# Kernel optimization log

Hardware: AMD Instinct MI355X
Metric: run time of the kernel (lower is better)

## Reference

```python
import jax, jax.numpy as jnp
import numpy as np

N = 32768
E = 524288
B = 128
D = 256


def setup_inputs() -> dict:
    key = jax.random.key(0)
    ks = jax.random.split(key, 8)
    b_z = jax.random.normal(ks[0], (N, D), dtype=jnp.float32)
    src = jax.random.randint(ks[1], (E,), 0, N, dtype=jnp.int32)
    dst = jax.random.randint(ks[2], (E,), 0, N, dtype=jnp.int32)
    b_edge_weight = jax.random.uniform(ks[3], (E,), dtype=jnp.float32)
    # Glorot-ish init for layer weights (256->128->64->1)
    W1 = jax.random.normal(ks[4], (256, 128), dtype=jnp.float32) / np.sqrt(256)
    W2 = jax.random.normal(ks[5], (128, 64), dtype=jnp.float32) / np.sqrt(128)
    W3 = jax.random.normal(ks[6], (64, 1), dtype=jnp.float32) / np.sqrt(64)
    b1 = jnp.zeros((128,), jnp.float32)
    b2 = jnp.zeros((64,), jnp.float32)
    b3 = jnp.zeros((1,), jnp.float32)
    return {"b_z": b_z, "src": src, "dst": dst, "b_edge_weight": b_edge_weight,
            "W1": W1, "b1": b1, "W2": W2, "b2": b2, "W3": W3, "b3": b3,
            "b_size": B}


def _degree_norms(src, dst, n):
    ones = jnp.ones(src.shape[0], jnp.float32)
    out_deg = jax.ops.segment_sum(ones, src, num_segments=n)
    in_deg = jax.ops.segment_sum(ones, dst, num_segments=n)
    # DGL GraphConv norm='both': unweighted degrees, clamped to 1
    return jnp.clip(out_deg, 1.0) ** -0.5, jnp.clip(in_deg, 1.0) ** -0.5


def _gcn_layer(x, src, dst, ew, norm_src, norm_dst, W, b, use_tanh):
    # norm='both': scale source features, transform first (in_feats > out_feats),
    # weighted neighbor sum, then scale by in-degree norm, add bias, activate.
    h = (x * norm_src[:, None]) @ W            # [N, out]
    m = h[src] * ew[:, None]                   # [E, out] gathered messages
    agg = jax.ops.segment_sum(m, dst, num_segments=x.shape[0])  # [N, out]
    out = agg * norm_dst[:, None] + b
    return jnp.tanh(out) if use_tanh else out


def reference(b_z, src, dst, b_edge_weight, W1, b1, W2, b2, W3, b3, b_size):
    norm_src, norm_dst = _degree_norms(src, dst, b_z.shape[0])
    h = _gcn_layer(b_z, src, dst, b_edge_weight, norm_src, norm_dst, W1, b1, True)
    h = _gcn_layer(h, src, dst, b_edge_weight, norm_src, norm_dst, W2, b2, True)
    h = _gcn_layer(h, src, dst, b_edge_weight, norm_src, norm_dst, W3, b3, False)
    return h.reshape(b_size, -1)
```

## Files before the change

kernel.cpp:

```cpp
#include <hip/hip_runtime.h>


#define NB 256
#define NW4 8192
#define RSEG 8

typedef unsigned int uint32;
typedef unsigned char uchar_t;
typedef unsigned short ushort_t;
typedef __attribute__((ext_vector_type(8))) short bf16x8;
typedef __attribute__((ext_vector_type(4))) float f32x4;

__device__ inline ushort_t f2bf(float f) {
  uint32 u = __float_as_uint(f);
  u += 0x7fffu + ((u >> 16) & 1u);
  return (ushort_t)(u >> 16);
}
__device__ inline float bf2f(ushort_t h) { return __uint_as_float(((uint32)h) << 16); }

__device__ inline float fast_tanh(float x) {
  float xc = fminf(fmaxf(x, -30.f), 30.f);
  float t = __expf(2.0f * xc);
  return (t - 1.0f) * __builtin_amdgcn_rcpf(t + 1.0f);
}

__global__ __launch_bounds__(1024) void hist_wsplit_kernel(
    const int* __restrict__ src, const int* __restrict__ dst, uint32* __restrict__ part,
    const float* __restrict__ W1, const float* __restrict__ W2,
    ushort_t* __restrict__ WhT1, ushort_t* __restrict__ WlT1,
    ushort_t* __restrict__ WhT2, int e, int epb) {
  const int t = threadIdx.x;
  if (blockIdx.x >= NB) {
    int i = (blockIdx.x - NB) * 1024 + t;
    if (i < 256 * 128) {
      int k = i / 128, c = i % 128;
      float f = W1[i];
      ushort_t h = f2bf(f);
      WhT1[(size_t)c * 256 + k] = h;
      WlT1[(size_t)c * 256 + k] = f2bf(f - bf2f(h));
    } else if (i < 256 * 128 + 128 * 64) {
      int j = i - 256 * 128;
      int k = j / 64, c = j % 64;
      WhT2[(size_t)c * 128 + k] = f2bf(W2[j]);
    }
    return;
  }
  __shared__ uint32 hs[NW4];
  __shared__ uint32 hd[NW4];
  for (int w = t; w < NW4; w += 1024) {
    hs[w] = 0;
    hd[w] = 0;
  }
  __syncthreads();
  const int base = blockIdx.x * epb;
  for (int k = t; k < epb; k += 1024) {
    int i = base + k;
    if (i < e) {
      int s = src[i], d = dst[i];
      atomicAdd(&hs[s >> 2], 1u << ((s & 3) * 8));
      atomicAdd(&hd[d >> 2], 1u << ((d & 3) * 8));
    }
  }
  __syncthreads();
  uint32* ps = part + (size_t)blockIdx.x * NW4;
  uint32* pd = part + (size_t)(NB + blockIdx.x) * NW4;
  for (int w = t; w < NW4; w += 1024) {
    ps[w] = hs[w];
    pd[w] = hd[w];
  }
}

__global__ __launch_bounds__(256) void norm_partial(const uint32* __restrict__ part,
                                                    uint32* __restrict__ psum, int n4) {
  const int w = blockIdx.x * 256 + threadIdx.x;
  const int seg = blockIdx.y;
  const int a = blockIdx.z;
  const uint32* p = part + (size_t)a * NB * n4 + (size_t)seg * (NB / RSEG) * n4 + w;
  uint32 s = 0;
#pragma unroll
  for (int r = 0; r < NB / RSEG; ++r) s += p[(size_t)r * n4];
  psum[(size_t)a * RSEG * n4 + (size_t)seg * n4 + w] = s;
}

__global__ __launch_bounds__(256) void norm_final(const uint32* __restrict__ psum,
                                                  float* __restrict__ norm_src,
                                                  float* __restrict__ norm_dst,
                                                  int* __restrict__ in_deg,
                                                  int* __restrict__ block_sums, int n4) {
  const int w = blockIdx.x * 256 + threadIdx.x;
  if (w >= n4) return;
  uint32 ss = 0, sd = 0;
#pragma unroll
  for (int seg = 0; seg < RSEG; ++seg) {
    ss += psum[(size_t)seg * n4 + w];
    sd += psum[(size_t)(RSEG + seg) * n4 + w];
  }
  int idsum = 0;
#pragma unroll
  for (int j = 0; j < 4; ++j) {
    int v = w * 4 + j;
    int od = (ss >> (j * 8)) & 0xff;
    int id = (sd >> (j * 8)) & 0xff;
    norm_src[v] = 1.0f / sqrtf((float)max(od, 1));
    norm_dst[v] = 1.0f / sqrtf((float)max(id, 1));
    in_deg[v] = id;
    idsum += id;
  }
#pragma unroll
  for (int off = 32; off > 0; off >>= 1) idsum += __shfl_down(idsum, off, 64);
  if ((threadIdx.x & 63) == 0) block_sums[w >> 6] = idsum;
}

__global__ __launch_bounds__(256) void scan_write_goffs(const int* __restrict__ in_deg,
                                                        const int* __restrict__ block_sums,
                                                        const uint32* __restrict__ part_dst,
                                                        int* __restrict__ row_ptr,
                                                        uchar_t* __restrict__ gpre, int n) {
  __shared__ int sh[256];
  __shared__ int s_boff;
  const int t = threadIdx.x;
  const int gid = blockIdx.x * 256 + t;
  {
    int v = (t < blockIdx.x && t < 128) ? block_sums[t] : 0;
#pragma unroll
    for (int off = 32; off > 0; off >>= 1) v += __shfl_down(v, off, 64);
    if ((t & 63) == 0) sh[t >> 6] = v;
    __syncthreads();
    if (t == 0) s_boff = sh[0] + sh[1] + sh[2] + sh[3];
    __syncthreads();
  }
  int d = (gid < n) ? in_deg[gid] : 0;
  sh[t] = d;
  __syncthreads();
  for (int off = 1; off < 256; off <<= 1) {
    int v = sh[t];
    int add = (t >= off) ? sh[t - off] : 0;
    __syncthreads();
    sh[t] = v + add;
    __syncthreads();
  }
  if (gid >= n) return;
  int excl = s_boff + sh[t] - d;
  row_ptr[gid] = excl;
  if (gid == n - 1) row_ptr[n] = excl + d;
  const int w = gid >> 2;
  const int shft = (gid & 3) * 8;
  const int n4 = n >> 2;
  int cum = 0;
#pragma unroll 8
  for (int r = 0; r < NB; ++r) {
    gpre[(size_t)r * n + gid] = (uchar_t)cum;
    cum += (part_dst[(size_t)r * n4 + w] >> shft) & 0xff;
  }
}

__global__ __launch_bounds__(1024) void scatter_kernel(const int* __restrict__ src,
                                                       const int* __restrict__ dst,
                                                       const float* __restrict__ ew,
                                                       const float* __restrict__ norm_src,
                                                       const int* __restrict__ row_ptr,
                                                       const uchar_t* __restrict__ gpre,
                                                       int2* __restrict__ csr,
                                                       int n, int e, int epb) {
  __shared__ uint32 rk[NW4];
  const int t = threadIdx.x;
  for (int w = t; w < NW4; w += 1024) rk[w] = 0;
  __syncthreads();
  const int base = blockIdx.x * epb;
  const uchar_t* gp = gpre + (size_t)blockIdx.x * n;
  for (int k = t; k < epb; k += 1024) {
    int i = base + k;
    if (i < e) {
      int s = src[i];
      int d = dst[i];
      uint32 sh = (d & 3) * 8;
      uint32 old = atomicAdd(&rk[d >> 2], 1u << sh);
      int rank = (old >> sh) & 0xff;
      int pos = row_ptr[d] + (int)gp[d] + rank;
      csr[pos] = make_int2(s, __float_as_int(ew[i] * norm_src[s]));
    }
  }
}

template <int K, int OUT>
__global__ __launch_bounds__(256) void gemm_mfma(const float* __restrict__ x,
                                                 const ushort_t* __restrict__ WhT,
                                                 const ushort_t* __restrict__ WlT,
                                                 ushort_t* __restrict__ ht, int n) {
  constexpr int BK = 64, KP = BK + 8;
  constexpr int NCT = OUT / 32;
  constexpr int NWLD = OUT * 16 / 256;
  __shared__ ushort_t Xh[64][KP];
  __shared__ ushort_t Wh[OUT][KP], Wl[OUT][KP];

  const int tid = threadIdx.x;
  const int wv = tid >> 6;
  const int lane = tid & 63;
  const int wr = wv >> 1;
  const int wc = wv & 1;
  const int row0 = blockIdx.x * 64;
  const int fr = lane & 15;
  const int fg = lane >> 4;

  f32x4 acc[2][NCT];
#pragma unroll
  for (int i = 0; i < 2; ++i)
#pragma unroll
    for (int j = 0; j < NCT; ++j) acc[i][j] = (f32x4){0.f, 0.f, 0.f, 0.f};

  float4 xr[4];
  ushort4 wrh[NWLD], wrl[NWLD];

#define LOADX(kg)                                                                       \
  {                                                                                     \
    _Pragma("unroll") for (int p_ = 0; p_ < 4; ++p_) {                                  \
      int idx_ = p_ * 256 + tid;                                                        \
      xr[p_] = *reinterpret_cast<const float4*>(                                        \
          x + (size_t)(row0 + (idx_ >> 4)) * K + (kg) + (idx_ & 15) * 4);               \
    }                                                                                   \
  }
#define LOADW(kg)                                                                       \
  {                                                                                     \
    _Pragma("unroll") for (int p_ = 0; p_ < NWLD; ++p_) {                               \
      int idx_ = p_ * 256 + tid;                                                        \
      int c_ = idx_ >> 4, k4_ = idx_ & 15;                                              \
      wrh[p_] = *reinterpret_cast<const ushort4*>(WhT + (size_t)c_ * K + (kg) + k4_ * 4);\
      wrl[p_] = *reinterpret_cast<const ushort4*>(WlT + (size_t)c_ * K + (kg) + k4_ * 4);\
    }                                                                                   \
  }

  LOADX(0);
  LOADW(0);

#pragma unroll 1
  for (int k0 = 0; k0 < K; k0 += BK) {
    __syncthreads();
#pragma unroll
    for (int p = 0; p < 4; ++p) {
      int idx = p * 256 + tid;
      int r = idx >> 4, c4 = idx & 15;
      float4 v = xr[p];
      ushort4 h;
      h.x = f2bf(v.x);
      h.y = f2bf(v.y);
      h.z = f2bf(v.z);
      h.w = f2bf(v.w);
      *reinterpret_cast<ushort4*>(&Xh[r][c4 * 4]) = h;
    }
#pragma unroll
    for (int p = 0; p < NWLD; ++p) {
      int idx = p * 256 + tid;
      int c = idx >> 4, k4 = idx & 15;
      *reinterpret_cast<ushort4*>(&Wh[c][k4 * 4]) = wrh[p];
      *reinterpret_cast<ushort4*>(&Wl[c][k4 * 4]) = wrl[p];
    }
    if (k0 + BK < K) {
      LOADX(k0 + BK);
      LOADW(k0 + BK);
    }
    __syncthreads();

#pragma unroll
    for (int s = 0; s < 2; ++s) {
      const int kk = s * 32 + fg * 8;
      bf16x8 ah[2];
#pragma unroll
      for (int i = 0; i < 2; ++i)
        ah[i] = *reinterpret_cast<const bf16x8*>(&Xh[wr * 32 + i * 16 + fr][kk]);
#pragma unroll
      for (int j = 0; j < NCT; ++j) {
        int c = wc * (OUT / 2) + j * 16 + fr;
        bf16x8 bh = *reinterpret_cast<const bf16x8*>(&Wh[c][kk]);
        bf16x8 bl = *reinterpret_cast<const bf16x8*>(&Wl[c][kk]);
#pragma unroll
        for (int i = 0; i < 2; ++i) {
          acc[i][j] = __builtin_amdgcn_mfma_f32_16x16x32_bf16(ah[i], bh, acc[i][j], 0, 0, 0);
          acc[i][j] = __builtin_amdgcn_mfma_f32_16x16x32_bf16(ah[i], bl, acc[i][j], 0, 0, 0);
        }
      }
    }
  }
#undef LOADX
#undef LOADW

#pragma unroll
  for (int i = 0; i < 2; ++i) {
#pragma unroll
    for (int q = 0; q < 4; ++q) {
      int row = row0 + wr * 32 + i * 16 + fg * 4 + q;
#pragma unroll
      for (int j = 0; j < NCT; ++j) {
        int col = wc * (OUT / 2) + j * 16 + fr;
        ht[(size_t)row * OUT + col] = f2bf(acc[i][j][q]);
      }
    }
  }
}

template <int K, int OUT>
__global__ __launch_bounds__(256) void gemm_mfma_bf16in(const ushort_t* __restrict__ x,
                                                        const ushort_t* __restrict__ WhT,
                                                        ushort_t* __restrict__ ht, int n) {
  constexpr int BK = 64, KP = BK + 8;
  constexpr int NCT = OUT / 32;
  constexpr int NWLD = OUT * 16 / 256;
  __shared__ ushort_t Xh[64][KP];
  __shared__ ushort_t Wh[OUT][KP];

  const int tid = threadIdx.x;
  const int wv = tid >> 6;
  const int lane = tid & 63;
  const int wr = wv >> 1;
  const int wc = wv & 1;
  const int row0 = blockIdx.x * 64;
  const int fr = lane & 15;
  const int fg = lane >> 4;

  f32x4 acc[2][NCT];
#pragma unroll
  for (int i = 0; i < 2; ++i)
#pragma unroll
    for (int j = 0; j < NCT; ++j) acc[i][j] = (f32x4){0.f, 0.f, 0.f, 0.f};

  ushort4 xr[4];
  ushort4 wrh[NWLD];

#define LOADX(kg)                                                                       \
  {                                                                                     \
    _Pragma("unroll") for (int p_ = 0; p_ < 4; ++p_) {                                  \
      int idx_ = p_ * 256 + tid;                                                        \
      xr[p_] = *reinterpret_cast<const ushort4*>(                                       \
          x + (size_t)(row0 + (idx_ >> 4)) * K + (kg) + (idx_ & 15) * 4);               \
    }                                                                                   \
  }
#define LOADW(kg)                                                                       \
  {                                                                                     \
    _Pragma("unroll") for (int p_ = 0; p_ < NWLD; ++p_) {                               \
      int idx_ = p_ * 256 + tid;                                                        \
      int c_ = idx_ >> 4, k4_ = idx_ & 15;                                              \
      wrh[p_] = *reinterpret_cast<const ushort4*>(WhT + (size_t)c_ * K + (kg) + k4_ * 4);\
    }                                                                                   \
  }

  LOADX(0);
  LOADW(0);

#pragma unroll 1
  for (int k0 = 0; k0 < K; k0 += BK) {
    __syncthreads();
#pragma unroll
    for (int p = 0; p < 4; ++p) {
      int idx = p * 256 + tid;
      *reinterpret_cast<ushort4*>(&Xh[idx >> 4][(idx & 15) * 4]) = xr[p];
    }
#pragma unroll
    for (int p = 0; p < NWLD; ++p) {
      int idx = p * 256 + tid;
      *reinterpret_cast<ushort4*>(&Wh[idx >> 4][(idx & 15) * 4]) = wrh[p];
    }
    if (k0 + BK < K) {
      LOADX(k0 + BK);
      LOADW(k0 + BK);
    }
    __syncthreads();

#pragma unroll
    for (int s = 0; s < 2; ++s) {
      const int kk = s * 32 + fg * 8;
      bf16x8 ah[2];
#pragma unroll
      for (int i = 0; i < 2; ++i)
        ah[i] = *reinterpret_cast<const bf16x8*>(&Xh[wr * 32 + i * 16 + fr][kk]);
#pragma unroll
      for (int j = 0; j < NCT; ++j) {
        int c = wc * (OUT / 2) + j * 16 + fr;
        bf16x8 bh = *reinterpret_cast<const bf16x8*>(&Wh[c][kk]);
#pragma unroll
        for (int i = 0; i < 2; ++i)
          acc[i][j] = __builtin_amdgcn_mfma_f32_16x16x32_bf16(ah[i], bh, acc[i][j], 0, 0, 0);
      }
    }
  }
#undef LOADX
#undef LOADW

#pragma unroll
  for (int i = 0; i < 2; ++i) {
#pragma unroll
    for (int q = 0; q < 4; ++q) {
      int row = row0 + wr * 32 + i * 16 + fg * 4 + q;
#pragma unroll
      for (int j = 0; j < NCT; ++j) {
        int col = wc * (OUT / 2) + j * 16 + fr;
        ht[(size_t)row * OUT + col] = f2bf(acc[i][j][q]);
      }
    }
  }
}

#define GATHB(e, acc)                                                               \
  {                                                                                 \
    float w_ = __int_as_float(e.y);                                                 \
    ushort4 h_ = *reinterpret_cast<const ushort4*>(ht + (size_t)e.x * OUT + cg * 4);\
    acc.x += w_ * bf2f(h_.x);                                                       \
    acc.y += w_ * bf2f(h_.y);                                                       \
    acc.z += w_ * bf2f(h_.z);                                                       \
    acc.w += w_ * bf2f(h_.w);                                                       \
  }

template <int OUT>
__global__ void aggregate_kernel(const ushort_t* __restrict__ ht, const int* __restrict__ row_ptr,
                                 const int2* __restrict__ csr, const float* __restrict__ norm_dst,
                                 const float* __restrict__ bias, ushort_t* __restrict__ out,
                                 int n) {
  constexpr int LPN = OUT / 4;
  constexpr int NPB = 256 / LPN;
  const int tid = threadIdx.x;
  const int cg = tid % LPN;
  const int v = blockIdx.x * NPB + tid / LPN;
  if (v >= n) return;

  const int s0 = row_ptr[v];
  const int s1 = row_ptr[v + 1];
  float4 a0 = {0, 0, 0, 0}, a1 = {0, 0, 0, 0}, a2 = {0, 0, 0, 0}, a3 = {0, 0, 0, 0};
  int i = s0;
  for (; i + 4 <= s1; i += 4) {
    int2 e0 = csr[i], e1 = csr[i + 1], e2 = csr[i + 2], e3 = csr[i + 3];
    GATHB(e0, a0);
    GATHB(e1, a1);
    GATHB(e2, a2);
    GATHB(e3, a3);
  }
  for (; i < s1; ++i) {
    int2 e = csr[i];
    GATHB(e, a0);
  }
  float nd = norm_dst[v];
  float4 b4 = *reinterpret_cast<const float4*>(bias + cg * 4);
  ushort4 r;
  r.x = f2bf(fast_tanh((a0.x + a1.x + a2.x + a3.x) * nd + b4.x));
  r.y = f2bf(fast_tanh((a0.y + a1.y + a2.y + a3.y) * nd + b4.y));
  r.z = f2bf(fast_tanh((a0.z + a1.z + a2.z + a3.z) * nd + b4.z));
  r.w = f2bf(fast_tanh((a0.w + a1.w + a2.w + a3.w) * nd + b4.w));
  *reinterpret_cast<ushort4*>(out + (size_t)v * OUT + cg * 4) = r;
}

__global__ void aggregate2_fuse3(const ushort_t* __restrict__ ht, const int* __restrict__ row_ptr,
                                 const int2* __restrict__ csr, const float* __restrict__ norm_dst,
                                 const float* __restrict__ bias, const float* __restrict__ W3,
                                 float* __restrict__ ht3, int n) {
  constexpr int OUT = 64;
  constexpr int LPN = OUT / 4;
  constexpr int NPB = 256 / LPN;
  const int tid = threadIdx.x;
  const int cg = tid % LPN;
  const int v = blockIdx.x * NPB + tid / LPN;
  if (v >= n) return;

  const int s0 = row_ptr[v];
  const int s1 = row_ptr[v + 1];
  float4 a0 = {0, 0, 0, 0}, a1 = {0, 0, 0, 0}, a2 = {0, 0, 0, 0}, a3 = {0, 0, 0, 0};
  int i = s0;
  for (; i + 4 <= s1; i += 4) {
    int2 e0 = csr[i], e1 = csr[i + 1], e2 = csr[i + 2], e3 = csr[i + 3];
    GATHB(e0, a0);
    GATHB(e1, a1);
    GATHB(e2, a2);
    GATHB(e3, a3);
  }
  for (; i < s1; ++i) {
    int2 e = csr[i];
    GATHB(e, a0);
  }
  float nd = norm_dst[v];
  float4 b4 = *reinterpret_cast<const float4*>(bias + cg * 4);
  float ox = fast_tanh((a0.x + a1.x + a2.x + a3.x) * nd + b4.x);
  float oy = fast_tanh((a0.y + a1.y + a2.y + a3.y) * nd + b4.y);
  float oz = fast_tanh((a0.z + a1.z + a2.z + a3.z) * nd + b4.z);
  float ow = fast_tanh((a0.w + a1.w + a2.w + a3.w) * nd + b4.w);
  float4 w3 = *reinterpret_cast<const float4*>(W3 + cg * 4);
  float p = ox * w3.x + oy * w3.y + oz * w3.z + ow * w3.w;
#pragma unroll
  for (int m = 1; m < 16; m <<= 1) p += __shfl_xor(p, m, 64);
  if (cg == 0) ht3[v] = p;
}

__global__ void aggregate3_kernel(const float* __restrict__ ht3, const int* __restrict__ row_ptr,
                                  const int2* __restrict__ csr, const float* __restrict__ norm_dst,
                                  const float* __restrict__ b3, float* __restrict__ out, int n) {
  int v = blockIdx.x * blockDim.x + threadIdx.x;
  if (v >= n) return;
  const int s0 = row_ptr[v];
  const int s1 = row_ptr[v + 1];
  float p0 = 0.f, p1 = 0.f, p2 = 0.f, p3 = 0.f;
  int i = s0;
  for (; i + 4 <= s1; i += 4) {
    int2 e0 = csr[i], e1 = csr[i + 1], e2 = csr[i + 2], e3 = csr[i + 3];
    p0 += __int_as_float(e0.y) * ht3[e0.x];
    p1 += __int_as_float(e1.y) * ht3[e1.x];
    p2 += __int_as_float(e2.y) * ht3[e2.x];
    p3 += __int_as_float(e3.y) * ht3[e3.x];
  }
  for (; i < s1; ++i) {
    int2 e = csr[i];
    p0 += __int_as_float(e.y) * ht3[e.x];
  }
  out[v] = (p0 + p1 + p2 + p3) * norm_dst[v] + b3[0];
}

extern "C" void kernel_launch(void* const* d_in, const int* in_sizes, int n_in,
                              void* d_out, int out_size, void* d_ws, size_t ws_size,
                              hipStream_t stream) {
  const float* b_z = (const float*)d_in[0];
  const int* src = (const int*)d_in[1];
  const int* dst = (const int*)d_in[2];
  const float* ew = (const float*)d_in[3];
  const float* W1 = (const float*)d_in[4];
  const float* b1 = (const float*)d_in[5];
  const float* W2 = (const float*)d_in[6];
  const float* b2 = (const float*)d_in[7];
  const float* W3 = (const float*)d_in[8];
  const float* b3 = (const float*)d_in[9];

  const int N = in_sizes[0] / 256;
  const int E = in_sizes[1];
  const int N4 = N / 4;
  const int epb = (E + NB - 1) / NB;

  char* ws = (char*)d_ws;
  size_t off = 0;
  auto alloc = [&](size_t bytes) -> void* {
    void* p = ws + off;
    off += (bytes + 255) & ~(size_t)255;
    return p;
  };

  uint32* part = (uint32*)alloc((size_t)2 * NB * N4 * 4);
  uint32* psum = (uint32*)alloc((size_t)2 * RSEG * N4 * 4);
  uchar_t* gpre = (uchar_t*)alloc((size_t)NB * N);
  float* norm_src = (float*)alloc((size_t)N * 4);
  float* norm_dst = (float*)alloc((size_t)N * 4);
  int* in_deg = (int*)alloc((size_t)N * 4);
  int* row_ptr = (int*)alloc((size_t)(N + 1) * 4);
  int* block_sums = (int*)alloc(256 * 4);
  int2* csr = (int2*)alloc((size_t)E * 8);
  ushort_t* HT = (ushort_t*)alloc((size_t)N * 128 * 2);
  ushort_t* ACT1 = (ushort_t*)alloc((size_t)N * 128 * 2);
  float* HT3 = (float*)alloc((size_t)N * 4);
  ushort_t* WhT1 = (ushort_t*)alloc((size_t)256 * 128 * 2);
  ushort_t* WlT1 = (ushort_t*)alloc((size_t)256 * 128 * 2);
  ushort_t* WhT2 = (ushort_t*)alloc((size_t)128 * 64 * 2);

  const uint32* part_dst = part + (size_t)NB * N4;
  const int nBlocks = (N + 255) / 256;
  const int wsBlocks = (256 * 128 + 128 * 64 + 1023) / 1024;

  hist_wsplit_kernel<<<NB + wsBlocks, 1024, 0, stream>>>(src, dst, part, W1, W2, WhT1, WlT1,
                                                         WhT2, E, epb);
  norm_partial<<<dim3(N4 / 256, RSEG, 2), 256, 0, stream>>>(part, psum, N4);
  norm_final<<<N4 / 256, 256, 0, stream>>>(psum, norm_src, norm_dst, in_deg, block_sums, N4);
  scan_write_goffs<<<nBlocks, 256, 0, stream>>>(in_deg, block_sums, part_dst, row_ptr, gpre, N);
  scatter_kernel<<<NB, 1024, 0, stream>>>(src, dst, ew, norm_src, row_ptr, gpre, csr, N, E, epb);

  gemm_mfma<256, 128><<<N / 64, 256, 0, stream>>>(b_z, WhT1, WlT1, HT, N);
  aggregate_kernel<128><<<(N + 7) / 8, 256, 0, stream>>>(HT, row_ptr, csr, norm_dst, b1, ACT1, N);
  gemm_mfma_bf16in<128, 64><<<N / 64, 256, 0, stream>>>(ACT1, WhT2, HT, N);
  aggregate2_fuse3<<<(N + 15) / 16, 256, 0, stream>>>(HT, row_ptr, csr, norm_dst, b2, W3, HT3, N);
  aggregate3_kernel<<<nBlocks, 256, 0, stream>>>(HT3, row_ptr, csr, norm_dst, b3,
                                                 (float*)d_out, N);
}
```

Before: 105.4 us.

## Fuse graph preprocessing kernels into one cooperative kernel with grid syncs

Measured after the change: 243.4 us. 131% more time.

```diff
diff --git a/kernel.cpp b/kernel.cpp
--- a/kernel.cpp
+++ b/kernel.cpp
@@ -1,4 +1,7 @@
 #include <hip/hip_runtime.h>
+#include <hip/hip_cooperative_groups.h>
+
+namespace cg = cooperative_groups;
 
 
 #define NB 256
@@ -24,160 +27,156 @@
   return (t - 1.0f) * __builtin_amdgcn_rcpf(t + 1.0f);
 }
 
-__global__ __launch_bounds__(1024) void hist_wsplit_kernel(
-    const int* __restrict__ src, const int* __restrict__ dst, uint32* __restrict__ part,
+__global__ __launch_bounds__(1024, 8) void preproc_coop(
+    const int* __restrict__ src, const int* __restrict__ dst, const float* __restrict__ ew,
     const float* __restrict__ W1, const float* __restrict__ W2,
-    ushort_t* __restrict__ WhT1, ushort_t* __restrict__ WlT1,
-    ushort_t* __restrict__ WhT2, int e, int epb) {
+    ushort_t* __restrict__ WhT1, ushort_t* __restrict__ WlT1, ushort_t* __restrict__ WhT2,
+    uint32* __restrict__ part, uint32* __restrict__ psum,
+    float* __restrict__ norm_src, float* __restrict__ norm_dst, int* __restrict__ in_deg,
+    int* __restrict__ block_sums, int* __restrict__ row_ptr, uchar_t* __restrict__ gpre,
+    int2* __restrict__ csr, int n, int e, int epb) {
+  cg::grid_group grid = cg::this_grid();
+  __shared__ uint32 hs[NW4];
+  __shared__ uint32 hd[NW4];
   const int t = threadIdx.x;
-  if (blockIdx.x >= NB) {
-    int i = (blockIdx.x - NB) * 1024 + t;
-    if (i < 256 * 128) {
-      int k = i / 128, c = i % 128;
-      float f = W1[i];
+  const int b = blockIdx.x;
+  const int n4 = n >> 2;
+
+  for (int w = t; w < NW4; w += 1024) {
+    hs[w] = 0;
+    hd[w] = 0;
+  }
+  __syncthreads();
+  {
+    const int base = b * epb;
+    for (int k = t; k < epb; k += 1024) {
+      int i = base + k;
+      if (i < e) {
+        int s = src[i], d = dst[i];
+        atomicAdd(&hs[s >> 2], 1u << ((s & 3) * 8));
+        atomicAdd(&hd[d >> 2], 1u << ((d & 3) * 8));
+      }
+    }
+    __syncthreads();
+    uint32* ps = part + (size_t)b * NW4;
+    uint32* pd = part + (size_t)(NB + b) * NW4;
+    for (int w = t; w < NW4; w += 1024) {
+      ps[w] = hs[w];
+      pd[w] = hd[w];
+    }
+    int j = b * 1024 + t;
+    if (j < 256 * 128) {
+      int k = j / 128, c = j % 128;
+      float f = W1[j];
       ushort_t h = f2bf(f);
       WhT1[(size_t)c * 256 + k] = h;
       WlT1[(size_t)c * 256 + k] = f2bf(f - bf2f(h));
-    } else if (i < 256 * 128 + 128 * 64) {
-      int j = i - 256 * 128;
-      int k = j / 64, c = j % 64;
-      WhT2[(size_t)c * 128 + k] = f2bf(W2[j]);
-    }
-    return;
-  }
-  __shared__ uint32 hs[NW4];
-  __shared__ uint32 hd[NW4];
-  for (int w = t; w < NW4; w += 1024) {
-    hs[w] = 0;
-    hd[w] = 0;
-  }
-  __syncthreads();
-  const int base = blockIdx.x * epb;
-  for (int k = t; k < epb; k += 1024) {
-    int i = base + k;
-    if (i < e) {
-      int s = src[i], d = dst[i];
-      atomicAdd(&hs[s >> 2], 1u << ((s & 3) * 8));
-      atomicAdd(&hd[d >> 2], 1u << ((d & 3) * 8));
-    }
-  }
-  __syncthreads();
-  uint32* ps = part + (size_t)blockIdx.x * NW4;
-  uint32* pd = part + (size_t)(NB + blockIdx.x) * NW4;
-  for (int w = t; w < NW4; w += 1024) {
-    ps[w] = hs[w];
-    pd[w] = hd[w];
-  }
-}
-
-__global__ __launch_bounds__(256) void norm_partial(const uint32* __restrict__ part,
-                                                    uint32* __restrict__ psum, int n4) {
-  const int w = blockIdx.x * 256 + threadIdx.x;
-  const int seg = blockIdx.y;
-  const int a = blockIdx.z;
-  const uint32* p = part + (size_t)a * NB * n4 + (size_t)seg * (NB / RSEG) * n4 + w;
-  uint32 s = 0;
-#pragma unroll
-  for (int r = 0; r < NB / RSEG; ++r) s += p[(size_t)r * n4];
-  psum[(size_t)a * RSEG * n4 + (size_t)seg * n4 + w] = s;
-}
-
-__global__ __launch_bounds__(256) void norm_final(const uint32* __restrict__ psum,
-                                                  float* __restrict__ norm_src,
-                                                  float* __restrict__ norm_dst,
-                                                  int* __restrict__ in_deg,
-                                                  int* __restrict__ block_sums, int n4) {
-  const int w = blockIdx.x * 256 + threadIdx.x;
-  if (w >= n4) return;
-  uint32 ss = 0, sd = 0;
-#pragma unroll
-  for (int seg = 0; seg < RSEG; ++seg) {
-    ss += psum[(size_t)seg * n4 + w];
-    sd += psum[(size_t)(RSEG + seg) * n4 + w];
-  }
-  int idsum = 0;
-#pragma unroll
-  for (int j = 0; j < 4; ++j) {
-    int v = w * 4 + j;
-    int od = (ss >> (j * 8)) & 0xff;
-    int id = (sd >> (j * 8)) & 0xff;
-    norm_src[v] = 1.0f / sqrtf((float)max(od, 1));
-    norm_dst[v] = 1.0f / sqrtf((float)max(id, 1));
-    in_deg[v] = id;
-    idsum += id;
-  }
-#pragma unroll
-  for (int off = 32; off > 0; off >>= 1) idsum += __shfl_down(idsum, off, 64);
-  if ((threadIdx.x & 63) == 0) block_sums[w >> 6] = idsum;
-}
-
-__global__ __launch_bounds__(256) void scan_write_goffs(const int* __restrict__ in_deg,
-                                                        const int* __restrict__ block_sums,
-                                                        const uint32* __restrict__ part_dst,
-                                                        int* __restrict__ row_ptr,
-                                                        uchar_t* __restrict__ gpre, int n) {
-  __shared__ int sh[256];
-  __shared__ int s_boff;
-  const int t = threadIdx.x;
-  const int gid = blockIdx.x * 256 + t;
+    } else if (j < 256 * 128 + 128 * 64) {
+      int jj = j - 256 * 128;
+      int k = jj / 64, c = jj % 64;
+      WhT2[(size_t)c * 128 + k] = f2bf(W2[jj]);
+    }
+  }
+  grid.sync();
+
   {
-    int v = (t < blockIdx.x && t < 128) ? block_sums[t] : 0;
+    int task = b * 1024 + t;
+    const int ntask = 2 * RSEG * n4;
+    if (task < ntask) {
+      int a = task / (RSEG * n4);
+      int rem = task % (RSEG * n4);
+      int seg = rem / n4;
+      int w = rem % n4;
+      const uint32* p = part + (size_t)a * NB * n4 + (size_t)seg * (NB / RSEG) * n4 + w;
+      uint32 s = 0;
+#pragma unroll
+      for (int r = 0; r < NB / RSEG; ++r) s += p[(size_t)r * n4];
+      psum[task] = s;
+    }
+  }
+  grid.sync();
+
+  if (b < 32 && t < 256) {
+    int w = b * 256 + t;
+    uint32 ss = 0, sd = 0;
+#pragma unroll
+    for (int seg = 0; seg < RSEG; ++seg) {
+      ss += psum[(size_t)seg * n4 + w];
+      sd += psum[(size_t)(RSEG + seg) * n4 + w];
+    }
+    int idsum = 0;
+#pragma unroll
+    for (int j = 0; j < 4; ++j) {
+      int v = w * 4 + j;
+      int od = (ss >> (j * 8)) & 0xff;
+      int id = (sd >> (j * 8)) & 0xff;
+      norm_src[v] = 1.0f / sqrtf((float)max(od, 1));
+      norm_dst[v] = 1.0f / sqrtf((float)max(id, 1));
+      in_deg[v] = id;
+      idsum += id;
+    }
+#pragma unroll
+    for (int off = 32; off > 0; off >>= 1) idsum += __shfl_down(idsum, off, 64);
+    if ((t & 63) == 0) block_sums[w >> 6] = idsum;
+  }
+  grid.sync();
+
+  {
+    int* sh = (int*)hs;
+    const bool act = (b < 128);
+    const int gid = b * 256 + (t & 255);
+    int v = (act && t < b && t < 128) ? block_sums[t] : 0;
 #pragma unroll
     for (int off = 32; off > 0; off >>= 1) v += __shfl_down(v, off, 64);
-    if ((t & 63) == 0) sh[t >> 6] = v;
-    __syncthreads();
-    if (t == 0) s_boff = sh[0] + sh[1] + sh[2] + sh[3];
-    __syncthreads();
-  }
-  int d = (gid < n) ? in_deg[gid] : 0;
-  sh[t] = d;
-  __syncthreads();
-  for (int off = 1; off < 256; off <<= 1) {
-    int v = sh[t];
-    int add = (t >= off) ? sh[t - off] : 0;
-    __syncthreads();
-    sh[t] = v + add;
-    __syncthreads();
-  }
-  if (gid >= n) return;
-  int excl = s_boff + sh[t] - d;
-  row_ptr[gid] = excl;
-  if (gid == n - 1) row_ptr[n] = excl + d;
-  const int w = gid >> 2;
-  const int shft = (gid & 3) * 8;
-  const int n4 = n >> 2;
-  int cum = 0;
+    if ((t & 63) == 0) sh[512 + (t >> 6)] = v;
+    __syncthreads();
+    const int s_boff = sh[512] + sh[513];
+    __syncthreads();
+    int d = (act && t < 256 && gid < n) ? in_deg[gid] : 0;
+    if (t < 256) sh[t] = d;
+    __syncthreads();
+    for (int off = 1; off < 256; off <<= 1) {
+      int vv = 0, add = 0;
+      if (t < 256) {
+        vv = sh[t];
+        add = (t >= off) ? sh[t - off] : 0;
+      }
+      __syncthreads();
+      if (t < 256) sh[t] = vv + add;
+      __syncthreads();
+    }
+    if (act && t < 256 && gid < n) {
+      int excl = s_boff + sh[t] - d;
+      row_ptr[gid] = excl;
+      if (gid == n - 1) row_ptr[n] = excl + d;
+      const int w = gid >> 2;
+      const int shft = (gid & 3) * 8;
+      int cum = 0;
 #pragma unroll 8
-  for (int r = 0; r < NB; ++r) {
-    gpre[(size_t)r * n + gid] = (uchar_t)cum;
-    cum += (part_dst[(size_t)r * n4 + w] >> shft) & 0xff;
-  }
-}
-
-__global__ __launch_bounds__(1024) void scatter_kernel(const int* __restrict__ src,
-                                                       const int* __restrict__ dst,
-                                                       const float* __restrict__ ew,
-                                                       const float* __restrict__ norm_src,
-                                                       const int* __restrict__ row_ptr,
-                                                       const uchar_t* __restrict__ gpre,
-                                                       int2* __restrict__ csr,
-                                                       int n, int e, int epb) {
-  __shared__ uint32 rk[NW4];
-  const int t = threadIdx.x;
-  for (int w = t; w < NW4; w += 1024) rk[w] = 0;
-  __syncthreads();
-  const int base = blockIdx.x * epb;
-  const uchar_t* gp = gpre + (size_t)blockIdx.x * n;
-  for (int k = t; k < epb; k += 1024) {
-    int i = base + k;
-    if (i < e) {
-      int s = src[i];
-      int d = dst[i];
-      uint32 sh = (d & 3) * 8;
-      uint32 old = atomicAdd(&rk[d >> 2], 1u << sh);
-      int rank = (old >> sh) & 0xff;
-      int pos = row_ptr[d] + (int)gp[d] + rank;
-      csr[pos] = make_int2(s, __float_as_int(ew[i] * norm_src[s]));
+      for (int r = 0; r < NB; ++r) {
+        gpre[(size_t)r * n + gid] = (uchar_t)cum;
+        cum += (part[(size_t)(NB + r) * n4 + w] >> shft) & 0xff;
+      }
+    }
+  }
+  grid.sync();
+
+  {
+    for (int w = t; w < NW4; w += 1024) hs[w] = 0;
+    __syncthreads();
+    const int base = b * epb;
+    const uchar_t* gp = gpre + (size_t)b * n;
+    for (int k = t; k < epb; k += 1024) {
+      int i = base + k;
+      if (i < e) {
+        int s = src[i];
+        int d = dst[i];
+        uint32 sh2 = (d & 3) * 8;
+        uint32 old = atomicAdd(&hs[d >> 2], 1u << sh2);
+        int rank = (old >> sh2) & 0xff;
+        int pos = row_ptr[d] + (int)gp[d] + rank;
+        csr[pos] = make_int2(s, __float_as_int(ew[i] * norm_src[s]));
+      }
     }
   }
 }
@@ -551,16 +550,15 @@
   ushort_t* WlT1 = (ushort_t*)alloc((size_t)256 * 128 * 2);
   ushort_t* WhT2 = (ushort_t*)alloc((size_t)128 * 64 * 2);
 
-  const uint32* part_dst = part + (size_t)NB * N4;
   const int nBlocks = (N + 255) / 256;
-  const int wsBlocks = (256 * 128 + 128 * 64 + 1023) / 1024;
-
-  hist_wsplit_kernel<<<NB + wsBlocks, 1024, 0, stream>>>(src, dst, part, W1, W2, WhT1, WlT1,
-                                                         WhT2, E, epb);
-  norm_partial<<<dim3(N4 / 256, RSEG, 2), 256, 0, stream>>>(part, psum, N4);
-  norm_final<<<N4 / 256, 256, 0, stream>>>(psum, norm_src, norm_dst, in_deg, block_sums, N4);
-  scan_write_goffs<<<nBlocks, 256, 0, stream>>>(in_deg, block_sums, part_dst, row_ptr, gpre, N);
-  scatter_kernel<<<NB, 1024, 0, stream>>>(src, dst, ew, norm_src, row_ptr, gpre, csr, N, E, epb);
+
+  int n_arg = N, e_arg = E, epb_arg = epb;
+  void* cargs[] = {(void*)&src,      (void*)&dst,        (void*)&ew,       (void*)&W1,
+                   (void*)&W2,       (void*)&WhT1,       (void*)&WlT1,     (void*)&WhT2,
+                   (void*)&part,     (void*)&psum,       (void*)&norm_src, (void*)&norm_dst,
+                   (void*)&in_deg,   (void*)&block_sums, (void*)&row_ptr,  (void*)&gpre,
+                   (void*)&csr,      (void*)&n_arg,      (void*)&e_arg,    (void*)&epb_arg};
+  hipLaunchCooperativeKernel((void*)preproc_coop, dim3(NB), dim3(1024), cargs, 0, stream);
 
   gemm_mfma<256, 128><<<N / 64, 256, 0, stream>>>(b_z, WhT1, WlT1, HT, N);
   aggregate_kernel<128><<<(N + 7) / 8, 256, 0, stream>>>(HT, row_ptr, csr, norm_dst, b1, ACT1, N);
```

## Fuse layer-1 aggregation with layer-2 GEMM into one kernel

Applied to the files above, without the earlier changes.

New measurement: 122.8 us. 16.4% more time.

```diff
diff --git a/kernel.cpp b/kernel.cpp
--- a/kernel.cpp
+++ b/kernel.cpp
@@ -126,7 +126,7 @@
     for (int off = 32; off > 0; off >>= 1) v += __shfl_down(v, off, 64);
     if ((t & 63) == 0) sh[t >> 6] = v;
     __syncthreads();
-    if (t == 0) s_boff = sh[0] + sh[1] + sh[2] + sh[3];
+    if (t == 0) s_boff = sh[0] + sh[1];
     __syncthreads();
   }
   int d = (gid < n) ? in_deg[gid] : 0;
@@ -297,123 +297,129 @@
   }
 }
 
-template <int K, int OUT>
-__global__ __launch_bounds__(256) void gemm_mfma_bf16in(const ushort_t* __restrict__ x,
-                                                        const ushort_t* __restrict__ WhT,
-                                                        ushort_t* __restrict__ ht, int n) {
-  constexpr int BK = 64, KP = BK + 8;
-  constexpr int NCT = OUT / 32;
-  constexpr int NWLD = OUT * 16 / 256;
-  __shared__ ushort_t Xh[64][KP];
-  __shared__ ushort_t Wh[OUT][KP];
+#define GATHB1(e, acc)                                                               \
+  {                                                                                  \
+    float w_ = __int_as_float(e.y);                                                  \
+    ushort4 h_ = *reinterpret_cast<const ushort4*>(ht + (size_t)e.x * 128 + cg * 4); \
+    acc.x += w_ * bf2f(h_.x);                                                        \
+    acc.y += w_ * bf2f(h_.y);                                                        \
+    acc.z += w_ * bf2f(h_.z);                                                        \
+    acc.w += w_ * bf2f(h_.w);                                                        \
+  }
+
+__global__ __launch_bounds__(256) void agg1_gemm2(const ushort_t* __restrict__ ht,
+                                                  const int* __restrict__ row_ptr,
+                                                  const int2* __restrict__ csr,
+                                                  const float* __restrict__ norm_dst,
+                                                  const float* __restrict__ b1,
+                                                  const ushort_t* __restrict__ WhT2,
+                                                  ushort_t* __restrict__ ht2, int n) {
+  constexpr int K = 128, OUT = 64, KP = K + 8;
+  __shared__ ushort_t ACT[64][KP];
+  __shared__ ushort_t WL[OUT][KP];
 
   const int tid = threadIdx.x;
+  const int v0 = blockIdx.x * 64;
+
+#pragma unroll
+  for (int p = 0; p < 8; ++p) {
+    int idx = p * 256 + tid;
+    int c = idx >> 5, k4 = idx & 31;
+    *reinterpret_cast<ushort4*>(&WL[c][k4 * 4]) =
+        *reinterpret_cast<const ushort4*>(WhT2 + (size_t)c * K + k4 * 4);
+  }
+
+  const int cg = tid & 31;
+  const int vsub = tid >> 5;
+#pragma unroll 1
+  for (int p = 0; p < 8; ++p) {
+    const int lv = p * 8 + vsub;
+    const int v = v0 + lv;
+    const int s0 = row_ptr[v];
+    const int s1 = row_ptr[v + 1];
+    float4 a0 = {0, 0, 0, 0}, a1 = {0, 0, 0, 0}, a2 = {0, 0, 0, 0}, a3 = {0, 0, 0, 0};
+    int i = s0;
+    for (; i + 4 <= s1; i += 4) {
+      int2 e0 = csr[i], e1 = csr[i + 1], e2 = csr[i + 2], e3 = csr[i + 3];
+      GATHB1(e0, a0);
+      GATHB1(e1, a1);
+      GATHB1(e2, a2);
+      GATHB1(e3, a3);
+    }
+    for (; i < s1; ++i) {
+      int2 e = csr[i];
+      GATHB1(e, a0);
+    }
+    float nd = norm_dst[v];
+    float4 b4 = *reinterpret_cast<const float4*>(b1 + cg * 4);
+    ushort4 r;
+    r.x = f2bf(fast_tanh((a0.x + a1.x + a2.x + a3.x) * nd + b4.x));
+    r.y = f2bf(fast_tanh((a0.y + a1.y + a2.y + a3.y) * nd + b4.y));
+    r.z = f2bf(fast_tanh((a0.z + a1.z + a2.z + a3.z) * nd + b4.z));
+    r.w = f2bf(fast_tanh((a0.w + a1.w + a2.w + a3.w) * nd + b4.w));
+    *reinterpret_cast<ushort4*>(&ACT[lv][cg * 4]) = r;
+  }
+  __syncthreads();
+
   const int wv = tid >> 6;
   const int lane = tid & 63;
   const int wr = wv >> 1;
   const int wc = wv & 1;
-  const int row0 = blockIdx.x * 64;
   const int fr = lane & 15;
   const int fg = lane >> 4;
 
-  f32x4 acc[2][NCT];
+  f32x4 acc[2][2];
 #pragma unroll
   for (int i = 0; i < 2; ++i)
 #pragma unroll
-    for (int j = 0; j < NCT; ++j) acc[i][j] = (f32x4){0.f, 0.f, 0.f, 0.f};
-
-  ushort4 xr[4];
-  ushort4 wrh[NWLD];
-
-#define LOADX(kg)                                                                       \
-  {                                                                                     \
-    _Pragma("unroll") for (int p_ = 0; p_ < 4; ++p_) {                                  \
-      int idx_ = p_ * 256 + tid;                                                        \
-      xr[p_] = *reinterpret_cast<const ushort4*>(                                       \
-          x + (size_t)(row0 + (idx_ >> 4)) * K + (kg) + (idx_ & 15) * 4);               \
-    }                                                                                   \
-  }
-#define LOADW(kg)                                                                       \
-  {                                                                                     \
-    _Pragma("unroll") for (int p_ = 0; p_ < NWLD; ++p_) {                               \
-      int idx_ = p_ * 256 + tid;                                                        \
-      int c_ = idx_ >> 4, k4_ = idx_ & 15;                                              \
-      wrh[p_] = *reinterpret_cast<const ushort4*>(WhT + (size_t)c_ * K + (kg) + k4_ * 4);\
-    }                                                                                   \
-  }
-
-  LOADX(0);
-  LOADW(0);
-
-#pragma unroll 1
-  for (int k0 = 0; k0 < K; k0 += BK) {
-    __syncthreads();
-#pragma unroll
-    for (int p = 0; p < 4; ++p) {
-      int idx = p * 256 + tid;
-      *reinterpret_cast<ushort4*>(&Xh[idx >> 4][(idx & 15) * 4]) = xr[p];
-    }
-#pragma unroll
-    for (int p = 0; p < NWLD; ++p) {
-      int idx = p * 256 + tid;
-      *reinterpret_cast<ushort4*>(&Wh[idx >> 4][(idx & 15) * 4]) = wrh[p];
-    }
-    if (k0 + BK < K) {
-      LOADX(k0 + BK);
-      LOADW(k0 + BK);
-    }
-    __syncthreads();
-
-#pragma unroll
-    for (int s = 0; s < 2; ++s) {
-      const int kk = s * 32 + fg * 8;
-      bf16x8 ah[2];
+    for (int j = 0; j < 2; ++j) acc[i][j] = (f32x4){0.f, 0.f, 0.f, 0.f};
+
+#pragma unroll
+  for (int s = 0; s < 4; ++s) {
+    const int kk = s * 32 + fg * 8;
+    bf16x8 ah[2];
+#pragma unroll
+    for (int i = 0; i < 2; ++i)
+      ah[i] = *reinterpret_cast<const bf16x8*>(&ACT[wr * 32 + i * 16 + fr][kk]);
+#pragma unroll
+    for (int j = 0; j < 2; ++j) {
+      int c = wc * 32 + j * 16 + fr;
+      bf16x8 bh = *reinterpret_cast<const bf16x8*>(&WL[c][kk]);
 #pragma unroll
       for (int i = 0; i < 2; ++i)
-        ah[i] = *reinterpret_cast<const bf16x8*>(&Xh[wr * 32 + i * 16 + fr][kk]);
-#pragma unroll
-      for (int j = 0; j < NCT; ++j) {
-        int c = wc * (OUT / 2) + j * 16 + fr;
-        bf16x8 bh = *reinterpret_cast<const bf16x8*>(&Wh[c][kk]);
-#pragma unroll
-        for (int i = 0; i < 2; ++i)
-          acc[i][j] = __builtin_amdgcn_mfma_f32_16x16x32_bf16(ah[i], bh, acc[i][j], 0, 0, 0);
+        acc[i][j] = __builtin_amdgcn_mfma_f32_16x16x32_bf16(ah[i], bh, acc[i][j], 0, 0, 0);
+    }
+  }
+
+#pragma unroll
+  for (int i = 0; i < 2; ++i) {
+#pragma unroll
+    for (int q = 0; q < 4; ++q) {
+      int row = v0 + wr * 32 + i * 16 + fg * 4 + q;
+#pragma unroll
+      for (int j = 0; j < 2; ++j) {
+        int col = wc * 32 + j * 16 + fr;
+        ht2[(size_t)row * OUT + col] = f2bf(acc[i][j][q]);
       }
     }
   }
-#undef LOADX
-#undef LOADW
-
-#pragma unroll
-  for (int i = 0; i < 2; ++i) {
-#pragma unroll
-    for (int q = 0; q < 4; ++q) {
-      int row = row0 + wr * 32 + i * 16 + fg * 4 + q;
-#pragma unroll
-      for (int j = 0; j < NCT; ++j) {
-        int col = wc * (OUT / 2) + j * 16 + fr;
-        ht[(size_t)row * OUT + col] = f2bf(acc[i][j][q]);
-      }
-    }
-  }
-}
-
-#define GATHB(e, acc)                                                               \
+}
+
+#define GATHB2(e, acc)                                                              \
   {                                                                                 \
     float w_ = __int_as_float(e.y);                                                 \
-    ushort4 h_ = *reinterpret_cast<const ushort4*>(ht + (size_t)e.x * OUT + cg * 4);\
+    ushort4 h_ = *reinterpret_cast<const ushort4*>(ht + (size_t)e.x * 64 + cg * 4); \
     acc.x += w_ * bf2f(h_.x);                                                       \
     acc.y += w_ * bf2f(h_.y);                                                       \
     acc.z += w_ * bf2f(h_.z);                                                       \
     acc.w += w_ * bf2f(h_.w);                                                       \
   }
 
-template <int OUT>
-__global__ void aggregate_kernel(const ushort_t* __restrict__ ht, const int* __restrict__ row_ptr,
+__global__ void aggregate2_fuse3(const ushort_t* __restrict__ ht, const int* __restrict__ row_ptr,
                                  const int2* __restrict__ csr, const float* __restrict__ norm_dst,
-                                 const float* __restrict__ bias, ushort_t* __restrict__ out,
-                                 int n) {
-  constexpr int LPN = OUT / 4;
+                                 const float* __restrict__ bias, const float* __restrict__ W3,
+                                 float* __restrict__ ht3, int n) {
+  constexpr int LPN = 16;
   constexpr int NPB = 256 / LPN;
   const int tid = threadIdx.x;
   const int cg = tid % LPN;
@@ -426,51 +432,14 @@
   int i = s0;
   for (; i + 4 <= s1; i += 4) {
     int2 e0 = csr[i], e1 = csr[i + 1], e2 = csr[i + 2], e3 = csr[i + 3];
-    GATHB(e0, a0);
-    GATHB(e1, a1);
-    GATHB(e2, a2);
-    GATHB(e3, a3);
+    GATHB2(e0, a0);
+    GATHB2(e1, a1);
+    GATHB2(e2, a2);
+    GATHB2(e3, a3);
   }
   for (; i < s1; ++i) {
     int2 e = csr[i];
-    GATHB(e, a0);
-  }
-  float nd = norm_dst[v];
-  float4 b4 = *reinterpret_cast<const float4*>(bias + cg * 4);
-  ushort4 r;
-  r.x = f2bf(fast_tanh((a0.x + a1.x + a2.x + a3.x) * nd + b4.x));
-  r.y = f2bf(fast_tanh((a0.y + a1.y + a2.y + a3.y) * nd + b4.y));
-  r.z = f2bf(fast_tanh((a0.z + a1.z + a2.z + a3.z) * nd + b4.z));
-  r.w = f2bf(fast_tanh((a0.w + a1.w + a2.w + a3.w) * nd + b4.w));
-  *reinterpret_cast<ushort4*>(out + (size_t)v * OUT + cg * 4) = r;
-}
-
-__global__ void aggregate2_fuse3(const ushort_t* __restrict__ ht, const int* __restrict__ row_ptr,
-                                 const int2* __restrict__ csr, const float* __restrict__ norm_dst,
-                                 const float* __restrict__ bias, const float* __restrict__ W3,
-                                 float* __restrict__ ht3, int n) {
-  constexpr int OUT = 64;
-  constexpr int LPN = OUT / 4;
-  constexpr int NPB = 256 / LPN;
-  const int tid = threadIdx.x;
-  const int cg = tid % LPN;
-  const int v = blockIdx.x * NPB + tid / LPN;
-  if (v >= n) return;
-
-  const int s0 = row_ptr[v];
-  const int s1 = row_ptr[v + 1];
-  float4 a0 = {0, 0, 0, 0}, a1 = {0, 0, 0, 0}, a2 = {0, 0, 0, 0}, a3 = {0, 0, 0, 0};
-  int i = s0;
-  for (; i + 4 <= s1; i += 4) {
-    int2 e0 = csr[i], e1 = csr[i + 1], e2 = csr[i + 2], e3 = csr[i + 3];
-    GATHB(e0, a0);
-    GATHB(e1, a1);
-    GATHB(e2, a2);
-    GATHB(e3, a3);
-  }
-  for (; i < s1; ++i) {
-    int2 e = csr[i];
-    GATHB(e, a0);
+    GATHB2(e, a0);
   }
   float nd = norm_dst[v];
   float4 b4 = *reinterpret_cast<const float4*>(bias + cg * 4);
@@ -544,8 +513,8 @@
   int* row_ptr = (int*)alloc((size_t)(N + 1) * 4);
   int* block_sums = (int*)alloc(256 * 4);
   int2* csr = (int2*)alloc((size_t)E * 8);
-  ushort_t* HT = (ushort_t*)alloc((size_t)N * 128 * 2);
-  ushort_t* ACT1 = (ushort_t*)alloc((size_t)N * 128 * 2);
+  ushort_t* HT1 = (ushort_t*)alloc((size_t)N * 128 * 2);
+  ushort_t* HT2 = (ushort_t*)alloc((size_t)N * 64 * 2);
   float* HT3 = (float*)alloc((size_t)N * 4);
   ushort_t* WhT1 = (ushort_t*)alloc((size_t)256 * 128 * 2);
   ushort_t* WlT1 = (ushort_t*)alloc((size_t)256 * 128 * 2);
@@ -562,10 +531,9 @@
   scan_write_goffs<<<nBlocks, 256, 0, stream>>>(in_deg, block_sums, part_dst, row_ptr, gpre, N);
   scatter_kernel<<<NB, 1024, 0, stream>>>(src, dst, ew, norm_src, row_ptr, gpre, csr, N, E, epb);
 
-  gemm_mfma<256, 128><<<N / 64, 256, 0, stream>>>(b_z, WhT1, WlT1, HT, N);
-  aggregate_kernel<128><<<(N + 7) / 8, 256, 0, stream>>>(HT, row_ptr, csr, norm_dst, b1, ACT1, N);
-  gemm_mfma_bf16in<128, 64><<<N / 64, 256, 0, stream>>>(ACT1, WhT2, HT, N);
-  aggregate2_fuse3<<<(N + 15) / 16, 256, 0, stream>>>(HT, row_ptr, csr, norm_dst, b2, W3, HT3, N);
+  gemm_mfma<256, 128><<<N / 64, 256, 0, stream>>>(b_z, WhT1, WlT1, HT1, N);
+  agg1_gemm2<<<N / 64, 256, 0, stream>>>(HT1, row_ptr, csr, norm_dst, b1, WhT2, HT2, N);
+  aggregate2_fuse3<<<(N + 15) / 16, 256, 0, stream>>>(HT2, row_ptr, csr, norm_dst, b2, W3, HT3, N);
   aggregate3_kernel<<<nBlocks, 256, 0, stream>>>(HT3, row_ptr, csr, norm_dst, b3,
                                                  (float*)d_out, N);
 }
```
